# Kernel optimization log

Hardware: AMD Instinct MI355X
Metric: run time of the kernel (lower is better)

Reference implementation:

```python
import jax, jax.numpy as jnp
import numpy as np

B, E, O, H = 4096, 1024, 16, 1024  # batch, embed_dim, num_ops, hidden_dim


def setup_inputs() -> dict:
    key = jax.random.key(0)
    k1, k2, k3, k4, k5, k6 = jax.random.split(key, 6)
    s1 = 1.0 / np.sqrt(E)
    s2 = 1.0 / np.sqrt(H)
    return {
        "x_aug": jax.random.normal(k1, (B, E), dtype=jnp.float32),
        "op_idx": jax.random.randint(k2, (B,), 0, O, dtype=jnp.int32),
        "W1": jax.random.normal(k3, (E, O, H), dtype=jnp.float32) * s1,  # DenseGeneral kernel: embed -> (ops, hidden)
        "b1": jnp.zeros((O, H), dtype=jnp.float32),
        "W2": jax.random.normal(k4, (H, O, H), dtype=jnp.float32) * s2,  # per-op second layer (diagonal of DenseGeneral)
        "b2": jnp.zeros((O, H), dtype=jnp.float32),
    }


def reference(x_aug, op_idx, W1, b1, W2, b2):
    # h1[b,o,h] = relu(sum_e x[b,e] W1[e,o,h] + b1[o,h])
    h1 = jax.nn.relu(jnp.einsum("be,eoh->boh", x_aug, W1) + b1)
    # h2[b,o,g] = relu(sum_h h1[b,o,h] W2[h,o,g] + b2[o,g])  (per-op MLP)
    h2 = jax.nn.relu(jnp.einsum("boh,hog->bog", h1, W2) + b2)
    # select the chosen operator's output per example
    idx = jnp.broadcast_to(op_idx[:, None, None], (x_aug.shape[0], 1, h2.shape[-1]))
    return jnp.take_along_axis(h2, idx, axis=1).squeeze(1)  # [B, H]
```

## Files before the change

kernel.cpp:

```cpp
#include <hip/hip_runtime.h>

#define Bn 4096
#define En 1024
#define On 16
#define Hn 1024
#define OHn (On * Hn)

#define BM 64
#define BN 128
#define BK 64

using floatx4 = __attribute__((ext_vector_type(4))) float;
using float4v = __attribute__((ext_vector_type(4))) float;
using bf16x8  = __attribute__((ext_vector_type(8))) __bf16;
using short8v = __attribute__((ext_vector_type(8))) short;

__device__ inline unsigned short f2bf(float f) {
    unsigned u = __builtin_bit_cast(unsigned, f);
    u += 0x7fffu + ((u >> 16) & 1u);
    return (unsigned short)(u >> 16);
}

__global__ void bucket_kernel(const int* __restrict__ op_idx,
                              int* __restrict__ sorted_idx,
                              int* __restrict__ offsets) {
    __shared__ int cnt[On], cur[On], off[On + 1];
    int tid = threadIdx.x;
    if (tid < On) { cnt[tid] = 0; cur[tid] = 0; }
    __syncthreads();
    for (int i = tid; i < Bn; i += blockDim.x) atomicAdd(&cnt[op_idx[i]], 1);
    __syncthreads();
    if (tid == 0) {
        int s = 0;
        for (int o = 0; o < On; ++o) { off[o] = s; s += cnt[o]; }
        off[On] = s;
    }
    __syncthreads();
    for (int i = tid; i < Bn; i += blockDim.x) {
        int o = op_idx[i];
        int p = off[o] + atomicAdd(&cur[o], 1);
        sorted_idx[p] = i;
    }
    if (tid <= On) offsets[tid] = off[tid];
}

__global__ __launch_bounds__(256) void gemm1_kernel(
    const float* __restrict__ x, const float* __restrict__ W1,
    const float* __restrict__ bias1, const int* __restrict__ sorted_idx,
    const int* __restrict__ offsets, unsigned short* __restrict__ h1) {
    int o = blockIdx.z;
    int off = offsets[o];
    int cnt = offsets[o + 1] - off;
    int m0 = blockIdx.y * BM;
    if (m0 >= cnt) return;
    int n0 = blockIdx.x * BN;

    __shared__ unsigned short As[8][BM][8];
    __shared__ unsigned short Bs[8][BN][8];

    int tid = threadIdx.x;

    int arow = tid & 63;
    int ag = tid >> 6;
    const float* aptr = nullptr;
    if (m0 + arow < cnt) aptr = x + (size_t)sorted_idx[off + m0 + arow] * En;

    int bn = tid & 127;
    int bg0 = (tid >> 7) * 4;
    const float* bptr = W1 + (size_t)o * Hn + n0 + bn;

    float a_pre[16] = {};
    float b_pre[32];

    floatx4 acc[2][4] = {};
    int lane = tid & 63;
    int wave = tid >> 6;
    int wm = (wave >> 1) * 32;
    int wn = (wave & 1) * 64;
    int l15 = lane & 15;
    int kg = lane >> 4;

#pragma unroll
    for (int i = 0; i < 2; ++i) {
        int k = (ag + 4 * i) * 8;
        if (aptr) {
            *(float4v*)&a_pre[i * 8]     = *(const float4v*)(aptr + k);
            *(float4v*)&a_pre[i * 8 + 4] = *(const float4v*)(aptr + k + 4);
        }
    }
#pragma unroll
    for (int g = 0; g < 4; ++g)
#pragma unroll
        for (int j = 0; j < 8; ++j)
            b_pre[g * 8 + j] = bptr[(size_t)((bg0 + g) * 8 + j) * OHn];

    for (int kt = 0; kt < En; kt += BK) {
#pragma unroll
        for (int i = 0; i < 2; ++i) {
            short8v v;
#pragma unroll
            for (int j = 0; j < 8; ++j) v[j] = (short)f2bf(a_pre[i * 8 + j]);
            *(short8v*)&As[ag + 4 * i][arow][0] = v;
        }
#pragma unroll
        for (int g = 0; g < 4; ++g) {
            short8v v;
#pragma unroll
            for (int j = 0; j < 8; ++j) v[j] = (short)f2bf(b_pre[g * 8 + j]);
            *(short8v*)&Bs[bg0 + g][bn][0] = v;
        }
        __syncthreads();

        int ktn = kt + BK;
        if (ktn < En) {
#pragma unroll
            for (int i = 0; i < 2; ++i) {
                int k = ktn + (ag + 4 * i) * 8;
                if (aptr) {
                    *(float4v*)&a_pre[i * 8]     = *(const float4v*)(aptr + k);
                    *(float4v*)&a_pre[i * 8 + 4] = *(const float4v*)(aptr + k + 4);
                }
            }
#pragma unroll
            for (int g = 0; g < 4; ++g)
#pragma unroll
                for (int j = 0; j < 8; ++j)
                    b_pre[g * 8 + j] = bptr[(size_t)(ktn + (bg0 + g) * 8 + j) * OHn];
        }

#pragma unroll
        for (int ks = 0; ks < 2; ++ks) {
            int g = ks * 4 + kg;
            bf16x8 af[2], bfr[4];
#pragma unroll
            for (int mt = 0; mt < 2; ++mt) af[mt] = *(const bf16x8*)&As[g][wm + mt * 16 + l15][0];
#pragma unroll
            for (int nt = 0; nt < 4; ++nt) bfr[nt] = *(const bf16x8*)&Bs[g][wn + nt * 16 + l15][0];
#pragma unroll
            for (int mt = 0; mt < 2; ++mt)
#pragma unroll
                for (int nt = 0; nt < 4; ++nt)
                    acc[mt][nt] = __builtin_amdgcn_mfma_f32_16x16x32_bf16(af[mt], bfr[nt], acc[mt][nt], 0, 0, 0);
        }
        __syncthreads();
    }

    int r4 = (lane >> 4) * 4;
#pragma unroll
    for (int nt = 0; nt < 4; ++nt) {
        int col = n0 + wn + nt * 16 + l15;
        float bv = bias1[o * Hn + col];
#pragma unroll
        for (int mt = 0; mt < 2; ++mt) {
#pragma unroll
            for (int r = 0; r < 4; ++r) {
                int row = m0 + wm + mt * 16 + r4 + r;
                if (row < cnt) {
                    float v = acc[mt][nt][r] + bv;
                    v = v > 0.f ? v : 0.f;
                    h1[(size_t)(off + row) * Hn + col] = f2bf(v);
                }
            }
        }
    }
}

__global__ __launch_bounds__(256) void gemm2_kernel(
    const unsigned short* __restrict__ h1, const float* __restrict__ W2,
    const float* __restrict__ bias2, const int* __restrict__ sorted_idx,
    const int* __restrict__ offsets, float* __restrict__ out) {
    int o = blockIdx.z;
    int off = offsets[o];
    int cnt = offsets[o + 1] - off;
    int m0 = blockIdx.y * BM;
    if (m0 >= cnt) return;
    int n0 = blockIdx.x * BN;

    __shared__ unsigned short As[8][BM][8];
    __shared__ unsigned short Bs[8][BN][8];

    int tid = threadIdx.x;

    int arow = tid & 63;
    int ag = tid >> 6;
    const unsigned short* aptr = nullptr;
    if (m0 + arow < cnt) aptr = h1 + (size_t)(off + m0 + arow) * Hn;

    int bn = tid & 127;
    int bg0 = (tid >> 7) * 4;
    const float* bptr = W2 + (size_t)o * Hn + n0 + bn;

    short8v a_pre[2] = {};
    float b_pre[32];

    floatx4 acc[2][4] = {};
    int lane = tid & 63;
    int wave = tid >> 6;
    int wm = (wave >> 1) * 32;
    int wn = (wave & 1) * 64;
    int l15 = lane & 15;
    int kg = lane >> 4;

#pragma unroll
    for (int i = 0; i < 2; ++i)
        if (aptr) a_pre[i] = *(const short8v*)(aptr + (ag + 4 * i) * 8);
#pragma unroll
    for (int g = 0; g < 4; ++g)
#pragma unroll
        for (int j = 0; j < 8; ++j)
            b_pre[g * 8 + j] = bptr[(size_t)((bg0 + g) * 8 + j) * OHn];

    for (int kt = 0; kt < Hn; kt += BK) {
#pragma unroll
        for (int i = 0; i < 2; ++i)
            *(short8v*)&As[ag + 4 * i][arow][0] = a_pre[i];
#pragma unroll
        for (int g = 0; g < 4; ++g) {
            short8v v;
#pragma unroll
            for (int j = 0; j < 8; ++j) v[j] = (short)f2bf(b_pre[g * 8 + j]);
            *(short8v*)&Bs[bg0 + g][bn][0] = v;
        }
        __syncthreads();

        int ktn = kt + BK;
        if (ktn < Hn) {
#pragma unroll
            for (int i = 0; i < 2; ++i)
                if (aptr) a_pre[i] = *(const short8v*)(aptr + ktn + (ag + 4 * i) * 8);
#pragma unroll
            for (int g = 0; g < 4; ++g)
#pragma unroll
                for (int j = 0; j < 8; ++j)
                    b_pre[g * 8 + j] = bptr[(size_t)(ktn + (bg0 + g) * 8 + j) * OHn];
        }

#pragma unroll
        for (int ks = 0; ks < 2; ++ks) {
            int g = ks * 4 + kg;
            bf16x8 af[2], bfr[4];
#pragma unroll
            for (int mt = 0; mt < 2; ++mt) af[mt] = *(const bf16x8*)&As[g][wm + mt * 16 + l15][0];
#pragma unroll
            for (int nt = 0; nt < 4; ++nt) bfr[nt] = *(const bf16x8*)&Bs[g][wn + nt * 16 + l15][0];
#pragma unroll
            for (int mt = 0; mt < 2; ++mt)
#pragma unroll
                for (int nt = 0; nt < 4; ++nt)
                    acc[mt][nt] = __builtin_amdgcn_mfma_f32_16x16x32_bf16(af[mt], bfr[nt], acc[mt][nt], 0, 0, 0);
        }
        __syncthreads();
    }

    int r4 = (lane >> 4) * 4;
    float bv[4];
#pragma unroll
    for (int nt = 0; nt < 4; ++nt) bv[nt] = bias2[o * Hn + n0 + wn + nt * 16 + l15];
#pragma unroll
    for (int mt = 0; mt < 2; ++mt) {
#pragma unroll
        for (int r = 0; r < 4; ++r) {
            int row = m0 + wm + mt * 16 + r4 + r;
            if (row < cnt) {
                int b = sorted_idx[off + row];
                float* orow = out + (size_t)b * Hn + n0 + wn + l15;
#pragma unroll
                for (int nt = 0; nt < 4; ++nt) {
                    float v = acc[mt][nt][r] + bv[nt];
                    orow[nt * 16] = v > 0.f ? v : 0.f;
                }
            }
        }
    }
}

extern "C" void kernel_launch(void* const* d_in, const int* in_sizes, int n_in,
                              void* d_out, int out_size, void* d_ws, size_t ws_size,
                              hipStream_t stream) {
    const float* x      = (const float*)d_in[0];
    const int*   op_idx = (const int*)d_in[1];
    const float* W1     = (const float*)d_in[2];
    const float* bias1  = (const float*)d_in[3];
    const float* W2     = (const float*)d_in[4];
    const float* bias2  = (const float*)d_in[5];
    float* out = (float*)d_out;

    char* ws = (char*)d_ws;
    int* offsets    = (int*)ws;
    int* sorted_idx = (int*)(ws + 256);
    unsigned short* h1 = (unsigned short*)(ws + 256 + 16384);

    hipLaunchKernelGGL(bucket_kernel, dim3(1), dim3(1024), 0, stream,
                       op_idx, sorted_idx, offsets);
    dim3 grid(Hn / BN, Bn / BM, On);
    hipLaunchKernelGGL(gemm1_kernel, grid, dim3(256), 0, stream,
                       x, W1, bias1, sorted_idx, offsets, h1);
    hipLaunchKernelGGL(gemm2_kernel, grid, dim3(256), 0, stream,
                       h1, W2, bias2, sorted_idx, offsets, out);
}
```

Baseline: 263.1 us.

## Pre-pack x and weights to bf16 k-grouped layout before grouped GEMMs

Adds pre-pass kernels that gather and convert the sorted x rows to bf16 and repack W1/W2 into a bf16 [op][k/8][h][8] layout, so the GEMM loops load contiguous 16-byte vectors with no per-tile fp32-to-bf16 conversion. This cuts global traffic and conversion work inside the main loops. In exchange it adds extra passes that read all of W1 and W2 on every call, plus a large workspace requirement. The old direct path is kept as a fallback when the workspace is too small.

```diff
diff --git a/kernel.cpp b/kernel.cpp
--- a/kernel.cpp
+++ b/kernel.cpp
@@ -14,6 +14,7 @@
 using float4v = __attribute__((ext_vector_type(4))) float;
 using bf16x8  = __attribute__((ext_vector_type(8))) __bf16;
 using short8v = __attribute__((ext_vector_type(8))) short;
+using short4v = __attribute__((ext_vector_type(4))) short;
 
 __device__ inline unsigned short f2bf(float f) {
     unsigned u = __builtin_bit_cast(unsigned, f);
@@ -44,7 +45,218 @@
     if (tid <= On) offsets[tid] = off[tid];
 }
 
+__global__ __launch_bounds__(256) void pack_x_kernel(const float* __restrict__ x,
+                                                     const int* __restrict__ sorted_idx,
+                                                     unsigned short* __restrict__ x_s) {
+    int p = blockIdx.x;
+    int row = sorted_idx[p];
+    int t = threadIdx.x;
+    float4v v = *(const float4v*)(x + (size_t)row * En + t * 4);
+    short4v w;
+#pragma unroll
+    for (int j = 0; j < 4; ++j) w[j] = (short)f2bf(v[j]);
+    *(short4v*)&x_s[(size_t)p * En + t * 4] = w;
+}
+
+__global__ __launch_bounds__(256) void pack_w_kernel(const float* __restrict__ W,
+                                                     unsigned short* __restrict__ Wp) {
+    int o = blockIdx.z;
+    int g = blockIdx.y;
+    int h = blockIdx.x * 256 + threadIdx.x;
+    const float* src = W + (size_t)(g * 8) * OHn + (size_t)o * Hn + h;
+    short8v v;
+#pragma unroll
+    for (int j = 0; j < 8; ++j) v[j] = (short)f2bf(src[(size_t)j * OHn]);
+    *(short8v*)&Wp[(((size_t)o * 128 + g) * Hn + h) * 8] = v;
+}
+
 __global__ __launch_bounds__(256) void gemm1_kernel(
+    const unsigned short* __restrict__ x_s, const unsigned short* __restrict__ Wp,
+    const float* __restrict__ bias1, const int* __restrict__ offsets,
+    unsigned short* __restrict__ h1) {
+    int o = blockIdx.z;
+    int off = offsets[o];
+    int cnt = offsets[o + 1] - off;
+    int m0 = blockIdx.y * BM;
+    if (m0 >= cnt) return;
+    int n0 = blockIdx.x * BN;
+
+    __shared__ unsigned short As[8][BM][8];
+    __shared__ unsigned short Bs[8][BN][8];
+
+    int tid = threadIdx.x;
+
+    int arow = tid & 63;
+    int ag = tid >> 6;
+    int rr0 = m0 + arow; if (rr0 >= cnt) rr0 = cnt - 1;
+    const unsigned short* aptr = x_s + (size_t)(off + rr0) * En;
+
+    int bn = tid & 127;
+    int bg = tid >> 7;
+    const unsigned short* bptr = Wp + (((size_t)o * 128 + bg) * Hn + n0 + bn) * 8;
+
+    short8v a_pre[2], b_pre[4];
+    floatx4 acc[2][4] = {};
+    int lane = tid & 63;
+    int wave = tid >> 6;
+    int wm = (wave >> 1) * 32;
+    int wn = (wave & 1) * 64;
+    int l15 = lane & 15;
+    int kg = lane >> 4;
+
+#pragma unroll
+    for (int i = 0; i < 2; ++i) a_pre[i] = *(const short8v*)(aptr + (ag + 4 * i) * 8);
+#pragma unroll
+    for (int i = 0; i < 4; ++i) b_pre[i] = *(const short8v*)(bptr + (size_t)i * (2 * Hn * 8));
+
+    for (int kt = 0; kt < En; kt += BK) {
+#pragma unroll
+        for (int i = 0; i < 2; ++i) *(short8v*)&As[ag + 4 * i][arow][0] = a_pre[i];
+#pragma unroll
+        for (int i = 0; i < 4; ++i) *(short8v*)&Bs[bg + 2 * i][bn][0] = b_pre[i];
+        __syncthreads();
+
+        int ktn = kt + BK;
+        if (ktn < En) {
+#pragma unroll
+            for (int i = 0; i < 2; ++i) a_pre[i] = *(const short8v*)(aptr + ktn + (ag + 4 * i) * 8);
+#pragma unroll
+            for (int i = 0; i < 4; ++i)
+                b_pre[i] = *(const short8v*)(bptr + (size_t)ktn * Hn + (size_t)i * (2 * Hn * 8));
+        }
+
+#pragma unroll
+        for (int ks = 0; ks < 2; ++ks) {
+            int g = ks * 4 + kg;
+            bf16x8 af[2], bfr[4];
+#pragma unroll
+            for (int mt = 0; mt < 2; ++mt) af[mt] = *(const bf16x8*)&As[g][wm + mt * 16 + l15][0];
+#pragma unroll
+            for (int nt = 0; nt < 4; ++nt) bfr[nt] = *(const bf16x8*)&Bs[g][wn + nt * 16 + l15][0];
+#pragma unroll
+            for (int mt = 0; mt < 2; ++mt)
+#pragma unroll
+                for (int nt = 0; nt < 4; ++nt)
+                    acc[mt][nt] = __builtin_amdgcn_mfma_f32_16x16x32_bf16(af[mt], bfr[nt], acc[mt][nt], 0, 0, 0);
+        }
+        __syncthreads();
+    }
+
+    int r4 = (lane >> 4) * 4;
+#pragma unroll
+    for (int nt = 0; nt < 4; ++nt) {
+        int col = n0 + wn + nt * 16 + l15;
+        float bv = bias1[o * Hn + col];
+#pragma unroll
+        for (int mt = 0; mt < 2; ++mt) {
+#pragma unroll
+            for (int r = 0; r < 4; ++r) {
+                int row = m0 + wm + mt * 16 + r4 + r;
+                if (row < cnt) {
+                    float v = acc[mt][nt][r] + bv;
+                    v = v > 0.f ? v : 0.f;
+                    h1[(size_t)(off + row) * Hn + col] = f2bf(v);
+                }
+            }
+        }
+    }
+}
+
+__global__ __launch_bounds__(256) void gemm2_kernel(
+    const unsigned short* __restrict__ h1, const unsigned short* __restrict__ Wp,
+    const float* __restrict__ bias2, const int* __restrict__ sorted_idx,
+    const int* __restrict__ offsets, float* __restrict__ out) {
+    int o = blockIdx.z;
+    int off = offsets[o];
+    int cnt = offsets[o + 1] - off;
+    int m0 = blockIdx.y * BM;
+    if (m0 >= cnt) return;
+    int n0 = blockIdx.x * BN;
+
+    __shared__ unsigned short As[8][BM][8];
+    __shared__ unsigned short Bs[8][BN][8];
+
+    int tid = threadIdx.x;
+
+    int arow = tid & 63;
+    int ag = tid >> 6;
+    int rr0 = m0 + arow; if (rr0 >= cnt) rr0 = cnt - 1;
+    const unsigned short* aptr = h1 + (size_t)(off + rr0) * Hn;
+
+    int bn = tid & 127;
+    int bg = tid >> 7;
+    const unsigned short* bptr = Wp + (((size_t)o * 128 + bg) * Hn + n0 + bn) * 8;
+
+    short8v a_pre[2], b_pre[4];
+    floatx4 acc[2][4] = {};
+    int lane = tid & 63;
+    int wave = tid >> 6;
+    int wm = (wave >> 1) * 32;
+    int wn = (wave & 1) * 64;
+    int l15 = lane & 15;
+    int kg = lane >> 4;
+
+#pragma unroll
+    for (int i = 0; i < 2; ++i) a_pre[i] = *(const short8v*)(aptr + (ag + 4 * i) * 8);
+#pragma unroll
+    for (int i = 0; i < 4; ++i) b_pre[i] = *(const short8v*)(bptr + (size_t)i * (2 * Hn * 8));
+
+    for (int kt = 0; kt < Hn; kt += BK) {
+#pragma unroll
+        for (int i = 0; i < 2; ++i) *(short8v*)&As[ag + 4 * i][arow][0] = a_pre[i];
+#pragma unroll
+        for (int i = 0; i < 4; ++i) *(short8v*)&Bs[bg + 2 * i][bn][0] = b_pre[i];
+        __syncthreads();
+
+        int ktn = kt + BK;
+        if (ktn < Hn) {
+#pragma unroll
+            for (int i = 0; i < 2; ++i) a_pre[i] = *(const short8v*)(aptr + ktn + (ag + 4 * i) * 8);
+#pragma unroll
+            for (int i = 0; i < 4; ++i)
+                b_pre[i] = *(const short8v*)(bptr + (size_t)ktn * Hn + (size_t)i * (2 * Hn * 8));
+        }
+
+#pragma unroll
+        for (int ks = 0; ks < 2; ++ks) {
+            int g = ks * 4 + kg;
+            bf16x8 af[2], bfr[4];
+#pragma unroll
+            for (int mt = 0; mt < 2; ++mt) af[mt] = *(const bf16x8*)&As[g][wm + mt * 16 + l15][0];
+#pragma unroll
+            for (int nt = 0; nt < 4; ++nt) bfr[nt] = *(const bf16x8*)&Bs[g][wn + nt * 16 + l15][0];
+#pragma unroll
+            for (int mt = 0; mt < 2; ++mt)
+#pragma unroll
+                for (int nt = 0; nt < 4; ++nt)
+                    acc[mt][nt] = __builtin_amdgcn_mfma_f32_16x16x32_bf16(af[mt], bfr[nt], acc[mt][nt], 0, 0, 0);
+        }
+        __syncthreads();
+    }
+
+    int r4 = (lane >> 4) * 4;
+    float bv[4];
+#pragma unroll
+    for (int nt = 0; nt < 4; ++nt) bv[nt] = bias2[o * Hn + n0 + wn + nt * 16 + l15];
+#pragma unroll
+    for (int mt = 0; mt < 2; ++mt) {
+#pragma unroll
+        for (int r = 0; r < 4; ++r) {
+            int row = m0 + wm + mt * 16 + r4 + r;
+            if (row < cnt) {
+                int b = sorted_idx[off + row];
+                float* orow = out + (size_t)b * Hn + n0 + wn + l15;
+#pragma unroll
+                for (int nt = 0; nt < 4; ++nt) {
+                    float v = acc[mt][nt][r] + bv[nt];
+                    orow[nt * 16] = v > 0.f ? v : 0.f;
+                }
+            }
+        }
+    }
+}
+
+__global__ __launch_bounds__(256) void gemm1_direct(
     const float* __restrict__ x, const float* __restrict__ W1,
     const float* __restrict__ bias1, const int* __restrict__ sorted_idx,
     const int* __restrict__ offsets, unsigned short* __restrict__ h1) {
@@ -59,7 +271,6 @@
     __shared__ unsigned short Bs[8][BN][8];
 
     int tid = threadIdx.x;
-
     int arow = tid & 63;
     int ag = tid >> 6;
     const float* aptr = nullptr;
@@ -165,7 +376,7 @@
     }
 }
 
-__global__ __launch_bounds__(256) void gemm2_kernel(
+__global__ __launch_bounds__(256) void gemm2_direct(
     const unsigned short* __restrict__ h1, const float* __restrict__ W2,
     const float* __restrict__ bias2, const int* __restrict__ sorted_idx,
     const int* __restrict__ offsets, float* __restrict__ out) {
@@ -180,7 +391,6 @@
     __shared__ unsigned short Bs[8][BN][8];
 
     int tid = threadIdx.x;
-
     int arow = tid & 63;
     int ag = tid >> 6;
     const unsigned short* aptr = nullptr;
@@ -288,13 +498,37 @@
     char* ws = (char*)d_ws;
     int* offsets    = (int*)ws;
     int* sorted_idx = (int*)(ws + 256);
-    unsigned short* h1 = (unsigned short*)(ws + 256 + 16384);
+
+    const size_t X_S_BYTES = (size_t)Bn * En * 2;
+    const size_t H1_BYTES  = (size_t)Bn * Hn * 2;
+    const size_t WP_BYTES  = (size_t)On * 128 * Hn * 8 * 2;
+    const size_t need = 16640 + X_S_BYTES + H1_BYTES + WP_BYTES;
 
     hipLaunchKernelGGL(bucket_kernel, dim3(1), dim3(1024), 0, stream,
                        op_idx, sorted_idx, offsets);
-    dim3 grid(Hn / BN, Bn / BM, On);
-    hipLaunchKernelGGL(gemm1_kernel, grid, dim3(256), 0, stream,
-                       x, W1, bias1, sorted_idx, offsets, h1);
-    hipLaunchKernelGGL(gemm2_kernel, grid, dim3(256), 0, stream,
-                       h1, W2, bias2, sorted_idx, offsets, out);
-}
+
+    if (ws_size >= need) {
+        unsigned short* x_s = (unsigned short*)(ws + 16640);
+        unsigned short* h1  = x_s + (size_t)Bn * En;
+        unsigned short* Wp  = h1 + (size_t)Bn * Hn;
+
+        dim3 grid(Hn / BN, Bn / BM, On);
+        hipLaunchKernelGGL(pack_x_kernel, dim3(Bn), dim3(256), 0, stream,
+                           x, sorted_idx, x_s);
+        hipLaunchKernelGGL(pack_w_kernel, dim3(Hn / 256, En / 8, On), dim3(256), 0, stream,
+                           W1, Wp);
+        hipLaunchKernelGGL(gemm1_kernel, grid, dim3(256), 0, stream,
+                           x_s, Wp, bias1, offsets, h1);
+        hipLaunchKernelGGL(pack_w_kernel, dim3(Hn / 256, Hn / 8, On), dim3(256), 0, stream,
+                           W2, Wp);
+        hipLaunchKernelGGL(gemm2_kernel, grid, dim3(256), 0, stream,
+                           h1, Wp, bias2, sorted_idx, offsets, out);
+    } else {
+        unsigned short* h1 = (unsigned short*)(ws + 256 + 16384);
+        dim3 grid(Hn / BN, Bn / BM, On);
+        hipLaunchKernelGGL(gemm1_direct, grid, dim3(256), 0, stream,
+                           x, W1, bias1, sorted_idx, offsets, h1);
+        hipLaunchKernelGGL(gemm2_direct, grid, dim3(256), 0, stream,
+                           h1, W2, bias2, sorted_idx, offsets, out);
+    }
+}
```

Result: faster. 257.8 us (-2.0%).

## Pre-pack weights and gathered activations to bf16, stage via global_load_lds double buffering

Applied to the files above, without the earlier changes.

Adds a pack pass that converts W1, W2 and the gathered x rows to bf16 in an MFMA-friendly interleaved layout. The GEMMs then load tiles directly into LDS with global_load_lds and double buffering. A compact tile list replaces the sparse per-op grid, so empty blocks are no longer launched. The cost is an extra full read and write of both weight tensors on every call, plus a larger workspace requirement, and nothing is launched if the workspace is too small.

```diff
diff --git a/kernel.cpp b/kernel.cpp
--- a/kernel.cpp
+++ b/kernel.cpp
@@ -9,11 +9,13 @@
 #define BM 64
 #define BN 128
 #define BK 64
+#define MAXT 80
 
 using floatx4 = __attribute__((ext_vector_type(4))) float;
 using float4v = __attribute__((ext_vector_type(4))) float;
 using bf16x8  = __attribute__((ext_vector_type(8))) __bf16;
 using short8v = __attribute__((ext_vector_type(8))) short;
+using short4v = __attribute__((ext_vector_type(4))) short;
 
 __device__ inline unsigned short f2bf(float f) {
     unsigned u = __builtin_bit_cast(unsigned, f);
@@ -21,9 +23,17 @@
     return (unsigned short)(u >> 16);
 }
 
+__device__ __forceinline__ void gld16(const unsigned short* g, unsigned short* l) {
+    __builtin_amdgcn_global_load_lds(
+        (const __attribute__((address_space(1))) unsigned int*)g,
+        (__attribute__((address_space(3))) unsigned int*)l, 16, 0, 0);
+}
+
 __global__ void bucket_kernel(const int* __restrict__ op_idx,
                               int* __restrict__ sorted_idx,
-                              int* __restrict__ offsets) {
+                              int* __restrict__ offsets,
+                              int* __restrict__ tile_o,
+                              int* __restrict__ tile_m) {
     __shared__ int cnt[On], cur[On], off[On + 1];
     int tid = threadIdx.x;
     if (tid < On) { cnt[tid] = 0; cur[tid] = 0; }
@@ -34,6 +44,10 @@
         int s = 0;
         for (int o = 0; o < On; ++o) { off[o] = s; s += cnt[o]; }
         off[On] = s;
+        int nt = 0;
+        for (int o = 0; o < On; ++o)
+            for (int m0 = 0; m0 < cnt[o]; m0 += BM) { tile_o[nt] = o; tile_m[nt] = m0; ++nt; }
+        for (; nt < MAXT; ++nt) { tile_o[nt] = -1; tile_m[nt] = 0; }
     }
     __syncthreads();
     for (int i = tid; i < Bn; i += blockDim.x) {
@@ -44,105 +58,118 @@
     if (tid <= On) offsets[tid] = off[tid];
 }
 
+__device__ __forceinline__ void pack_w_block(const float* __restrict__ W,
+                                             unsigned short* __restrict__ Wp,
+                                             int o, int g, int hblk, int t) {
+    int h = hblk * 256 + t;
+    const float* src = W + (size_t)(g * 8) * OHn + (size_t)o * Hn + h;
+    short8v v;
+#pragma unroll
+    for (int j = 0; j < 8; ++j) v[j] = (short)f2bf(src[(size_t)j * OHn]);
+    *(short8v*)&Wp[(((size_t)o * 128 + g) * Hn + h) * 8] = v;
+}
+
+__device__ __forceinline__ void pack_x_block(const float* __restrict__ x,
+                                             const int* __restrict__ sorted_idx,
+                                             unsigned short* __restrict__ x_s,
+                                             int p, int t) {
+    int row = sorted_idx[p];
+    float4v v = *(const float4v*)(x + (size_t)row * En + t * 4);
+    short4v w;
+#pragma unroll
+    for (int j = 0; j < 4; ++j) w[j] = (short)f2bf(v[j]);
+    *(short4v*)&x_s[(size_t)p * En + t * 4] = w;
+}
+
+__global__ __launch_bounds__(256) void pack_all_kernel(
+    const float* __restrict__ W1, const float* __restrict__ W2,
+    const float* __restrict__ x, const int* __restrict__ sorted_idx,
+    unsigned short* __restrict__ Wp1, unsigned short* __restrict__ Wp2,
+    unsigned short* __restrict__ x_s) {
+    int b = blockIdx.x, t = threadIdx.x;
+    if (b < 8192) {
+        pack_w_block(W1, Wp1, b >> 9, (b >> 2) & 127, b & 3, t);
+    } else if (b < 16384) {
+        int c = b - 8192;
+        pack_w_block(W2, Wp2, c >> 9, (c >> 2) & 127, c & 3, t);
+    } else {
+        pack_x_block(x, sorted_idx, x_s, b - 16384, t);
+    }
+}
+
+__global__ __launch_bounds__(256) void pack_x_kernel(const float* __restrict__ x,
+                                                     const int* __restrict__ sorted_idx,
+                                                     unsigned short* __restrict__ x_s) {
+    pack_x_block(x, sorted_idx, x_s, blockIdx.x, threadIdx.x);
+}
+__global__ __launch_bounds__(256) void pack_w_kernel(const float* __restrict__ W,
+                                                     unsigned short* __restrict__ Wp) {
+    pack_w_block(W, Wp, blockIdx.z, blockIdx.y, blockIdx.x, threadIdx.x);
+}
+
 __global__ __launch_bounds__(256) void gemm1_kernel(
-    const float* __restrict__ x, const float* __restrict__ W1,
-    const float* __restrict__ bias1, const int* __restrict__ sorted_idx,
-    const int* __restrict__ offsets, unsigned short* __restrict__ h1) {
-    int o = blockIdx.z;
+    const unsigned short* __restrict__ x_s, const unsigned short* __restrict__ Wp,
+    const float* __restrict__ bias1, const int* __restrict__ offsets,
+    const int* __restrict__ tile_o, const int* __restrict__ tile_m,
+    unsigned short* __restrict__ h1) {
+    int o = tile_o[blockIdx.y];
+    if (o < 0) return;
+    int m0 = tile_m[blockIdx.y];
     int off = offsets[o];
     int cnt = offsets[o + 1] - off;
-    int m0 = blockIdx.y * BM;
-    if (m0 >= cnt) return;
     int n0 = blockIdx.x * BN;
 
-    __shared__ unsigned short As[8][BM][8];
-    __shared__ unsigned short Bs[8][BN][8];
+    __shared__ __attribute__((aligned(16))) unsigned short As[2][8][BM][8];
+    __shared__ __attribute__((aligned(16))) unsigned short Bs[2][8][BN][8];
 
     int tid = threadIdx.x;
 
-    int arow = tid & 63;
-    int ag = tid >> 6;
-    const float* aptr = nullptr;
-    if (m0 + arow < cnt) aptr = x + (size_t)sorted_idx[off + m0 + arow] * En;
-
-    int bn = tid & 127;
-    int bg0 = (tid >> 7) * 4;
-    const float* bptr = W1 + (size_t)o * Hn + n0 + bn;
-
-    float a_pre[16] = {};
-    float b_pre[32];
+    int arow = tid & 63, ag = tid >> 6;
+    int rr = m0 + arow; if (rr >= cnt) rr = cnt - 1;
+    const unsigned short* aBase = x_s + (size_t)(off + rr) * En;
+
+    int bn = tid & 127, bg = tid >> 7;
+    const unsigned short* bBase = Wp + (((size_t)o * 128 + bg) * Hn + n0 + bn) * 8;
+
+    auto STAGE = [&](int buf, int kt) {
+        gld16(aBase + kt + ag * 8,        &As[buf][ag][arow][0]);
+        gld16(aBase + kt + (ag + 4) * 8,  &As[buf][ag + 4][arow][0]);
+        const unsigned short* bk = bBase + (size_t)kt * Hn;
+#pragma unroll
+        for (int i = 0; i < 4; ++i)
+            gld16(bk + (size_t)i * (2 * Hn * 8), &Bs[buf][bg + 2 * i][bn][0]);
+    };
 
     floatx4 acc[2][4] = {};
-    int lane = tid & 63;
-    int wave = tid >> 6;
-    int wm = (wave >> 1) * 32;
-    int wn = (wave & 1) * 64;
-    int l15 = lane & 15;
-    int kg = lane >> 4;
-
-#pragma unroll
-    for (int i = 0; i < 2; ++i) {
-        int k = (ag + 4 * i) * 8;
-        if (aptr) {
-            *(float4v*)&a_pre[i * 8]     = *(const float4v*)(aptr + k);
-            *(float4v*)&a_pre[i * 8 + 4] = *(const float4v*)(aptr + k + 4);
-        }
-    }
-#pragma unroll
-    for (int g = 0; g < 4; ++g)
-#pragma unroll
-        for (int j = 0; j < 8; ++j)
-            b_pre[g * 8 + j] = bptr[(size_t)((bg0 + g) * 8 + j) * OHn];
-
-    for (int kt = 0; kt < En; kt += BK) {
-#pragma unroll
-        for (int i = 0; i < 2; ++i) {
-            short8v v;
-#pragma unroll
-            for (int j = 0; j < 8; ++j) v[j] = (short)f2bf(a_pre[i * 8 + j]);
-            *(short8v*)&As[ag + 4 * i][arow][0] = v;
-        }
-#pragma unroll
-        for (int g = 0; g < 4; ++g) {
-            short8v v;
-#pragma unroll
-            for (int j = 0; j < 8; ++j) v[j] = (short)f2bf(b_pre[g * 8 + j]);
-            *(short8v*)&Bs[bg0 + g][bn][0] = v;
-        }
-        __syncthreads();
-
-        int ktn = kt + BK;
-        if (ktn < En) {
-#pragma unroll
-            for (int i = 0; i < 2; ++i) {
-                int k = ktn + (ag + 4 * i) * 8;
-                if (aptr) {
-                    *(float4v*)&a_pre[i * 8]     = *(const float4v*)(aptr + k);
-                    *(float4v*)&a_pre[i * 8 + 4] = *(const float4v*)(aptr + k + 4);
-                }
-            }
-#pragma unroll
-            for (int g = 0; g < 4; ++g)
-#pragma unroll
-                for (int j = 0; j < 8; ++j)
-                    b_pre[g * 8 + j] = bptr[(size_t)(ktn + (bg0 + g) * 8 + j) * OHn];
-        }
-
+    int lane = tid & 63, wave = tid >> 6;
+    int wm = (wave >> 1) * 32, wn = (wave & 1) * 64;
+    int l15 = lane & 15, kg = lane >> 4;
+
+    auto COMPUTE = [&](int buf) {
 #pragma unroll
         for (int ks = 0; ks < 2; ++ks) {
             int g = ks * 4 + kg;
             bf16x8 af[2], bfr[4];
 #pragma unroll
-            for (int mt = 0; mt < 2; ++mt) af[mt] = *(const bf16x8*)&As[g][wm + mt * 16 + l15][0];
-#pragma unroll
-            for (int nt = 0; nt < 4; ++nt) bfr[nt] = *(const bf16x8*)&Bs[g][wn + nt * 16 + l15][0];
+            for (int mt = 0; mt < 2; ++mt) af[mt] = *(const bf16x8*)&As[buf][g][wm + mt * 16 + l15][0];
+#pragma unroll
+            for (int nt = 0; nt < 4; ++nt) bfr[nt] = *(const bf16x8*)&Bs[buf][g][wn + nt * 16 + l15][0];
 #pragma unroll
             for (int mt = 0; mt < 2; ++mt)
 #pragma unroll
                 for (int nt = 0; nt < 4; ++nt)
                     acc[mt][nt] = __builtin_amdgcn_mfma_f32_16x16x32_bf16(af[mt], bfr[nt], acc[mt][nt], 0, 0, 0);
         }
+    };
+
+    STAGE(0, 0);
+    for (int kt = 0; kt < En; kt += 2 * BK) {
         __syncthreads();
+        STAGE(1, kt + BK);
+        COMPUTE(0);
+        __syncthreads();
+        if (kt + 2 * BK < En) STAGE(0, kt + 2 * BK);
+        COMPUTE(1);
     }
 
     int r4 = (lane >> 4) * 4;
@@ -166,90 +193,68 @@
 }
 
 __global__ __launch_bounds__(256) void gemm2_kernel(
-    const unsigned short* __restrict__ h1, const float* __restrict__ W2,
+    const unsigned short* __restrict__ h1, const unsigned short* __restrict__ Wp,
     const float* __restrict__ bias2, const int* __restrict__ sorted_idx,
-    const int* __restrict__ offsets, float* __restrict__ out) {
-    int o = blockIdx.z;
+    const int* __restrict__ offsets, const int* __restrict__ tile_o,
+    const int* __restrict__ tile_m, float* __restrict__ out) {
+    int o = tile_o[blockIdx.y];
+    if (o < 0) return;
+    int m0 = tile_m[blockIdx.y];
     int off = offsets[o];
     int cnt = offsets[o + 1] - off;
-    int m0 = blockIdx.y * BM;
-    if (m0 >= cnt) return;
     int n0 = blockIdx.x * BN;
 
-    __shared__ unsigned short As[8][BM][8];
-    __shared__ unsigned short Bs[8][BN][8];
+    __shared__ __attribute__((aligned(16))) unsigned short As[2][8][BM][8];
+    __shared__ __attribute__((aligned(16))) unsigned short Bs[2][8][BN][8];
 
     int tid = threadIdx.x;
 
-    int arow = tid & 63;
-    int ag = tid >> 6;
-    const unsigned short* aptr = nullptr;
-    if (m0 + arow < cnt) aptr = h1 + (size_t)(off + m0 + arow) * Hn;
-
-    int bn = tid & 127;
-    int bg0 = (tid >> 7) * 4;
-    const float* bptr = W2 + (size_t)o * Hn + n0 + bn;
-
-    short8v a_pre[2] = {};
-    float b_pre[32];
+    int arow = tid & 63, ag = tid >> 6;
+    int rr = m0 + arow; if (rr >= cnt) rr = cnt - 1;
+    const unsigned short* aBase = h1 + (size_t)(off + rr) * Hn;
+
+    int bn = tid & 127, bg = tid >> 7;
+    const unsigned short* bBase = Wp + (((size_t)o * 128 + bg) * Hn + n0 + bn) * 8;
+
+    auto STAGE = [&](int buf, int kt) {
+        gld16(aBase + kt + ag * 8,        &As[buf][ag][arow][0]);
+        gld16(aBase + kt + (ag + 4) * 8,  &As[buf][ag + 4][arow][0]);
+        const unsigned short* bk = bBase + (size_t)kt * Hn;
+#pragma unroll
+        for (int i = 0; i < 4; ++i)
+            gld16(bk + (size_t)i * (2 * Hn * 8), &Bs[buf][bg + 2 * i][bn][0]);
+    };
 
     floatx4 acc[2][4] = {};
-    int lane = tid & 63;
-    int wave = tid >> 6;
-    int wm = (wave >> 1) * 32;
-    int wn = (wave & 1) * 64;
-    int l15 = lane & 15;
-    int kg = lane >> 4;
-
-#pragma unroll
-    for (int i = 0; i < 2; ++i)
-        if (aptr) a_pre[i] = *(const short8v*)(aptr + (ag + 4 * i) * 8);
-#pragma unroll
-    for (int g = 0; g < 4; ++g)
-#pragma unroll
-        for (int j = 0; j < 8; ++j)
-            b_pre[g * 8 + j] = bptr[(size_t)((bg0 + g) * 8 + j) * OHn];
-
-    for (int kt = 0; kt < Hn; kt += BK) {
-#pragma unroll
-        for (int i = 0; i < 2; ++i)
-            *(short8v*)&As[ag + 4 * i][arow][0] = a_pre[i];
-#pragma unroll
-        for (int g = 0; g < 4; ++g) {
-            short8v v;
-#pragma unroll
-            for (int j = 0; j < 8; ++j) v[j] = (short)f2bf(b_pre[g * 8 + j]);
-            *(short8v*)&Bs[bg0 + g][bn][0] = v;
-        }
-        __syncthreads();
-
-        int ktn = kt + BK;
-        if (ktn < Hn) {
-#pragma unroll
-            for (int i = 0; i < 2; ++i)
-                if (aptr) a_pre[i] = *(const short8v*)(aptr + ktn + (ag + 4 * i) * 8);
-#pragma unroll
-            for (int g = 0; g < 4; ++g)
-#pragma unroll
-                for (int j = 0; j < 8; ++j)
-                    b_pre[g * 8 + j] = bptr[(size_t)(ktn + (bg0 + g) * 8 + j) * OHn];
-        }
-
+    int lane = tid & 63, wave = tid >> 6;
+    int wm = (wave >> 1) * 32, wn = (wave & 1) * 64;
+    int l15 = lane & 15, kg = lane >> 4;
+
+    auto COMPUTE = [&](int buf) {
 #pragma unroll
         for (int ks = 0; ks < 2; ++ks) {
             int g = ks * 4 + kg;
             bf16x8 af[2], bfr[4];
 #pragma unroll
-            for (int mt = 0; mt < 2; ++mt) af[mt] = *(const bf16x8*)&As[g][wm + mt * 16 + l15][0];
-#pragma unroll
-            for (int nt = 0; nt < 4; ++nt) bfr[nt] = *(const bf16x8*)&Bs[g][wn + nt * 16 + l15][0];
+            for (int mt = 0; mt < 2; ++mt) af[mt] = *(const bf16x8*)&As[buf][g][wm + mt * 16 + l15][0];
+#pragma unroll
+            for (int nt = 0; nt < 4; ++nt) bfr[nt] = *(const bf16x8*)&Bs[buf][g][wn + nt * 16 + l15][0];
 #pragma unroll
             for (int mt = 0; mt < 2; ++mt)
 #pragma unroll
                 for (int nt = 0; nt < 4; ++nt)
                     acc[mt][nt] = __builtin_amdgcn_mfma_f32_16x16x32_bf16(af[mt], bfr[nt], acc[mt][nt], 0, 0, 0);
         }
+    };
+
+    STAGE(0, 0);
+    for (int kt = 0; kt < Hn; kt += 2 * BK) {
         __syncthreads();
+        STAGE(1, kt + BK);
+        COMPUTE(0);
+        __syncthreads();
+        if (kt + 2 * BK < Hn) STAGE(0, kt + 2 * BK);
+        COMPUTE(1);
     }
 
     int r4 = (lane >> 4) * 4;
@@ -288,13 +293,42 @@
     char* ws = (char*)d_ws;
     int* offsets    = (int*)ws;
     int* sorted_idx = (int*)(ws + 256);
-    unsigned short* h1 = (unsigned short*)(ws + 256 + 16384);
+    int* tile_o     = (int*)(ws + 16640);
+    int* tile_m     = (int*)(ws + 17152);
+
+    const size_t HDR       = 32768;
+    const size_t X_S_ELEMS = (size_t)Bn * En;
+    const size_t H1_ELEMS  = (size_t)Bn * Hn;
+    const size_t WP_ELEMS  = (size_t)On * 128 * Hn * 8;
+    const size_t need_full = HDR + 2 * (X_S_ELEMS + H1_ELEMS + WP_ELEMS);
+    const size_t need_half = HDR + 2 * (X_S_ELEMS + H1_ELEMS + WP_ELEMS) - 2 * WP_ELEMS;
+
+    unsigned short* x_s = (unsigned short*)(ws + HDR);
+    unsigned short* h1  = x_s + X_S_ELEMS;
+    unsigned short* Wp1 = h1 + H1_ELEMS;
+    unsigned short* Wp2 = Wp1 + WP_ELEMS;
 
     hipLaunchKernelGGL(bucket_kernel, dim3(1), dim3(1024), 0, stream,
-                       op_idx, sorted_idx, offsets);
-    dim3 grid(Hn / BN, Bn / BM, On);
-    hipLaunchKernelGGL(gemm1_kernel, grid, dim3(256), 0, stream,
-                       x, W1, bias1, sorted_idx, offsets, h1);
-    hipLaunchKernelGGL(gemm2_kernel, grid, dim3(256), 0, stream,
-                       h1, W2, bias2, sorted_idx, offsets, out);
-}
+                       op_idx, sorted_idx, offsets, tile_o, tile_m);
+
+    dim3 grid_g(Hn / BN, MAXT);
+    if (ws_size >= need_full) {
+        hipLaunchKernelGGL(pack_all_kernel, dim3(20480), dim3(256), 0, stream,
+                           W1, W2, x, sorted_idx, Wp1, Wp2, x_s);
+        hipLaunchKernelGGL(gemm1_kernel, grid_g, dim3(256), 0, stream,
+                           x_s, Wp1, bias1, offsets, tile_o, tile_m, h1);
+        hipLaunchKernelGGL(gemm2_kernel, grid_g, dim3(256), 0, stream,
+                           h1, Wp2, bias2, sorted_idx, offsets, tile_o, tile_m, out);
+    } else if (ws_size >= need_half) {
+        hipLaunchKernelGGL(pack_x_kernel, dim3(Bn), dim3(256), 0, stream,
+                           x, sorted_idx, x_s);
+        hipLaunchKernelGGL(pack_w_kernel, dim3(Hn / 256, En / 8, On), dim3(256), 0, stream,
+                           W1, Wp1);
+        hipLaunchKernelGGL(gemm1_kernel, grid_g, dim3(256), 0, stream,
+                           x_s, Wp1, bias1, offsets, tile_o, tile_m, h1);
+        hipLaunchKernelGGL(pack_w_kernel, dim3(Hn / 256, Hn / 8, On), dim3(256), 0, stream,
+                           W2, Wp1);
+        hipLaunchKernelGGL(gemm2_kernel, grid_g, dim3(256), 0, stream,
+                           h1, Wp1, bias2, sorted_idx, offsets, tile_o, tile_m, out);
+    }
+}
```

Result: faster. 241.5 us (-8.2%).
